# Kernel optimization log

Hardware: AMD Instinct MI355X
Metric: run time of the kernel (lower is better)

Reference implementation:

```python
import jax, jax.numpy as jnp
import numpy as np

N_NODES = 50000
N_EDGES = 800000
IN_CH = 128
HID_CH = 512
OUT_CH = 256


def setup_inputs() -> dict:
    key = jax.random.key(0)
    k1, k2, k3, k4, k5, k6 = jax.random.split(key, 6)
    x = jax.random.normal(k1, (N_NODES, IN_CH), dtype=jnp.float32)
    edge_index = jnp.stack([
        jax.random.randint(k2, (N_EDGES,), 0, N_NODES, dtype=jnp.int64),
        jax.random.randint(k3, (N_EDGES,), 0, N_NODES, dtype=jnp.int64),
    ], axis=0)
    # Xavier-uniform init as in MLP.reset_parameters
    lim1 = float(np.sqrt(6.0 / (IN_CH + HID_CH)))
    lim2 = float(np.sqrt(6.0 / (HID_CH + OUT_CH)))
    W1 = jax.random.uniform(k4, (IN_CH, HID_CH), jnp.float32, -lim1, lim1)
    b1 = jnp.zeros((HID_CH,), jnp.float32)
    W2 = jax.random.uniform(k5, (HID_CH, OUT_CH), jnp.float32, -lim2, lim2)
    return {"x": x, "edge_index": edge_index, "W1": W1, "b1": b1, "W2": W2}


def reference(x, edge_index, W1, b1, W2):
    src = edge_index[0]
    dst = edge_index[1]
    # AnisoConv (K=None): unweighted SpMM with adj.t() -> out[dst] += x[src]
    agg = jax.ops.segment_sum(x[src], dst, num_segments=N_NODES)  # [N, in_ch]
    h = agg + x  # residual add of x_r = x[:size[1]] = x
    # MLP: Linear(in, hidden, bias=True) -> Linear(hidden, out, bias=False)
    h = h @ W1 + b1
    h = h @ W2
    return h
```

## Files before the change

### kernel.cpp

```cpp
#include <hip/hip_runtime.h>

#define N_NODES 50000
#define N_EDGES 800000
#define IN_CH   128
#define HID_CH  512
#define OUT_CH  256

#define BKT_SHIFT 7
#define BKT_NODES 128
#define NBKT ((N_NODES + BKT_NODES - 1) / BKT_NODES)
#define BCAP 4096
#define P1_EPT    8
#define P1_EPB    (512 * P1_EPT)
#define P1_BLOCKS ((N_EDGES + P1_EPB - 1) / P1_EPB)
#define CVT_BLOCKS 3125

typedef __attribute__((ext_vector_type(8))) short bf16x8;
typedef __attribute__((ext_vector_type(4))) float f32x4;

static __device__ __forceinline__ ushort f2bf(float f) {
    uint u = __float_as_uint(f);
    uint r = u + 0x7fffu + ((u >> 16) & 1u);
    return (ushort)(r >> 16);
}

__global__ __launch_bounds__(1024) void build_w12(const float* __restrict__ W1,
                                                  const float* __restrict__ b1,
                                                  const float* __restrict__ W2,
                                                  ushort* __restrict__ W12t,
                                                  float* __restrict__ b2,
                                                  int* __restrict__ bucketcnt) {
    __shared__ float a[4][HID_CH];
    __shared__ float red[4][4][256];
    const int t   = threadIdx.x;
    const int j   = t & 255;
    const int kc  = t >> 8;
    const int blk = blockIdx.x;
    if (blk == 0 && t < NBKT) bucketcnt[t] = 0;

    const bool bias = (blk == 32);
    if (!bias) {
        const int i0 = blk * 4;
        for (int lin = t; lin < 4 * HID_CH; lin += 1024)
            a[lin >> 9][lin & 511] = W1[(size_t)(i0 + (lin >> 9)) * HID_CH + (lin & 511)];
    } else {
        for (int lin = t; lin < HID_CH; lin += 1024) a[0][lin] = b1[lin];
    }
    __syncthreads();

    float acc[4] = {0.f, 0.f, 0.f, 0.f};
    const int k0 = kc * 128;
    if (!bias) {
        for (int k = k0; k < k0 + 128; ++k) {
            const float w = W2[(size_t)k * OUT_CH + j];
#pragma unroll
            for (int r = 0; r < 4; ++r) acc[r] = fmaf(a[r][k], w, acc[r]);
        }
    } else {
        for (int k = k0; k < k0 + 128; ++k)
            acc[0] = fmaf(a[0][k], W2[(size_t)k * OUT_CH + j], acc[0]);
    }
#pragma unroll
    for (int r = 0; r < 4; ++r) red[kc][r][j] = acc[r];
    __syncthreads();
    if (kc == 0) {
#pragma unroll
        for (int r = 0; r < 4; ++r) {
            const float s = red[0][r][j] + red[1][r][j] + red[2][r][j] + red[3][r][j];
            if (!bias) W12t[(size_t)j * IN_CH + blk * 4 + r] = f2bf(s);
            else if (r == 0) b2[j] = s;
        }
    }
}

__global__ __launch_bounds__(512) void cvt_part(const float* __restrict__ x,
                                                ushort* __restrict__ xb,
                                                const int* __restrict__ ei,
                                                int* __restrict__ bucketcnt,
                                                uint* __restrict__ pairbuf) {
    __shared__ uint stage[P1_EPB];
    __shared__ int cnt[512], off[512], cur[512], base[512];
    const int t = threadIdx.x;

    if (blockIdx.x < CVT_BLOCKS) {
        const int gid = blockIdx.x * 512 + t;
        const float4 v = *(const float4*)(x + (size_t)gid * 4);
        ushort4 o;
        o.x = f2bf(v.x); o.y = f2bf(v.y); o.z = f2bf(v.z); o.w = f2bf(v.w);
        *(ushort4*)(xb + (size_t)gid * 4) = o;
        return;
    }

    const int e0 = (blockIdx.x - CVT_BLOCKS) * P1_EPB;

    cnt[t] = 0;
    __syncthreads();

    uint pk[P1_EPT];
    int  bk[P1_EPT];
    bool vl[P1_EPT];
#pragma unroll
    for (int i = 0; i < P1_EPT; ++i) {
        const int e = e0 + i * 512 + t;
        vl[i] = (e < N_EDGES);
        if (vl[i]) {
            const int src = ei[e];
            const int dst = ei[N_EDGES + e];
            const int b = dst >> BKT_SHIFT;
            bk[i] = b;
            pk[i] = ((uint)b << 23) | ((uint)src << 7) | (uint)(dst & (BKT_NODES - 1));
            atomicAdd(&cnt[b], 1);
        }
    }
    __syncthreads();

    off[t] = cnt[t];
    __syncthreads();
#pragma unroll
    for (int d = 1; d < 512; d <<= 1) {
        const int u = (t >= d) ? off[t - d] : 0;
        __syncthreads();
        off[t] += u;
        __syncthreads();
    }
    off[t] -= cnt[t];
    cur[t] = off[t];
    if (t < NBKT && cnt[t] > 0)
        base[t] = t * BCAP + atomicAdd(&bucketcnt[t], cnt[t]);
    __syncthreads();

#pragma unroll
    for (int i = 0; i < P1_EPT; ++i)
        if (vl[i]) {
            const int lp = atomicAdd(&cur[bk[i]], 1);
            stage[lp] = pk[i];
        }
    __syncthreads();

    const int TOT = off[511] + cnt[511];
    for (int idx = t; idx < TOT; idx += 512) {
        const uint p = stage[idx];
        const int b = (int)(p >> 23);
        pairbuf[base[b] + (idx - off[b])] = p;
    }
}

__global__ __launch_bounds__(256) void bucket_fill2(const uint* __restrict__ pairbuf,
                                                    const int* __restrict__ bucketcnt,
                                                    int* __restrict__ locrow,
                                                    int* __restrict__ srcidx) {
    __shared__ int cnt[128], off[128], cur[128];
    const int b = blockIdx.x;
    const int t = threadIdx.x;
    const int ne = bucketcnt[b];
    const uint* eb = pairbuf + (size_t)b * BCAP;

    if (t < 128) cnt[t] = 0;
    __syncthreads();
    for (int i = t; i < ne; i += 256)
        atomicAdd(&cnt[eb[i] & (BKT_NODES - 1)], 1);
    __syncthreads();

    if (t < 128) off[t] = cnt[t];
    __syncthreads();
#pragma unroll
    for (int d = 1; d < 128; d <<= 1) {
        int u = 0;
        if (t < 128 && t >= d) u = off[t - d];
        __syncthreads();
        if (t < 128 && t >= d) off[t] += u;
        __syncthreads();
    }
    if (t < 128) {
        off[t] -= cnt[t];
        cur[t] = off[t];
        locrow[b * (BKT_NODES + 1) + t] = off[t];
        if (t == 0) locrow[b * (BKT_NODES + 1) + BKT_NODES] = ne;
    }
    __syncthreads();

    for (int i = t; i < ne; i += 256) {
        const uint p = eb[i];
        const int ln  = (int)(p & (BKT_NODES - 1));
        const int src = (int)((p >> 7) & 0xFFFFu);
        const int pos = atomicAdd(&cur[ln], 1);
        srcidx[(size_t)b * BCAP + pos] = src;
    }
}

__global__ __launch_bounds__(256) void gather_bf16(const ushort* __restrict__ xb,
                                                   const int* __restrict__ locrow,
                                                   const int* __restrict__ srcidx,
                                                   ushort* __restrict__ aggb) {
    const int node = (int)((blockIdx.x * 256u + threadIdx.x) >> 6);
    const int lane = threadIdx.x & 63;
    if (node >= N_NODES) return;
    const int b  = node >> BKT_SHIFT;
    const int ln = node & (BKT_NODES - 1);
    const uint* xrow = (const uint*)xb;
    const uint self = xrow[(size_t)node * 64 + lane];
    float ax = __uint_as_float(self << 16);
    float ay = __uint_as_float(self & 0xffff0000u);
    int e = locrow[b * (BKT_NODES + 1) + ln];
    const int end = locrow[b * (BKT_NODES + 1) + ln + 1];
    const int* sb = srcidx + (size_t)b * BCAP;
    for (; e + 8 <= end; e += 8) {
        uint v[8];
#pragma unroll
        for (int i = 0; i < 8; ++i) {
            const int s = sb[e + i];
            v[i] = xrow[(size_t)s * 64 + lane];
        }
#pragma unroll
        for (int i = 0; i < 8; ++i) {
            ax += __uint_as_float(v[i] << 16);
            ay += __uint_as_float(v[i] & 0xffff0000u);
        }
    }
    for (; e < end; ++e) {
        const uint v = xrow[(size_t)sb[e] * 64 + lane];
        ax += __uint_as_float(v << 16); ay += __uint_as_float(v & 0xffff0000u);
    }
    const uint packed = ((uint)f2bf(ay) << 16) | (uint)f2bf(ax);
    ((uint*)aggb)[(size_t)node * 64 + lane] = packed;
}

__global__ __launch_bounds__(512) void mfma_gemm(const ushort* __restrict__ aggb,
                                                 const ushort* __restrict__ w12t,
                                                 const float* __restrict__ b2,
                                                 float* __restrict__ out) {
    __shared__ ushort bt[256 * 128];
    const int tid = threadIdx.x;

#pragma unroll
    for (int it = 0; it < 8; ++it) {
        const int i = tid + it * 512;
        const int n = i >> 4, s = i & 15;
        const uint4 v = *(const uint4*)(w12t + (size_t)i * 8);
        *(uint4*)(&bt[(n << 7) + ((s ^ (n & 7)) << 3)]) = v;
    }
    __syncthreads();

    const int lane = tid & 63;
    const int w    = tid >> 6;
    const int rbase = blockIdx.x * 128 + (w >> 1) * 32;
    const int cbase = (w & 1) * 128;
    const int l15 = lane & 15;
    const int oct = lane >> 4;

    f32x4 acc[2][8];
#pragma unroll
    for (int m = 0; m < 2; ++m)
#pragma unroll
        for (int n = 0; n < 8; ++n)
            acc[m][n] = (f32x4){0.f, 0.f, 0.f, 0.f};

#pragma unroll
    for (int kk = 0; kk < 4; ++kk) {
        bf16x8 afr[2];
#pragma unroll
        for (int m = 0; m < 2; ++m) {
            int row = rbase + m * 16 + l15;
            row = row < N_NODES ? row : N_NODES - 1;
            afr[m] = *(const bf16x8*)(aggb + (size_t)row * IN_CH + kk * 32 + oct * 8);
        }
#pragma unroll
        for (int n = 0; n < 8; ++n) {
            const int col  = cbase + n * 16 + l15;
            const int slot = (kk * 4 + oct) ^ (col & 7);
            const bf16x8 bfr = *(const bf16x8*)(&bt[(col << 7) + (slot << 3)]);
#pragma unroll
            for (int m = 0; m < 2; ++m)
                acc[m][n] = __builtin_amdgcn_mfma_f32_16x16x32_bf16(
                    afr[m], bfr, acc[m][n], 0, 0, 0);
        }
    }

#pragma unroll
    for (int m = 0; m < 2; ++m) {
        const int row0 = rbase + m * 16 + oct * 4;
#pragma unroll
        for (int n = 0; n < 8; ++n) {
            const int col = cbase + n * 16 + l15;
            const float bias = b2[col];
#pragma unroll
            for (int r = 0; r < 4; ++r) {
                const int row = row0 + r;
                if (row < N_NODES)
                    __builtin_nontemporal_store(acc[m][n][r] + bias,
                                                &out[(size_t)row * OUT_CH + col]);
            }
        }
    }
}

extern "C" void kernel_launch(void* const* d_in, const int* in_sizes, int n_in,
                              void* d_out, int out_size, void* d_ws, size_t ws_size,
                              hipStream_t stream) {
    const float* x  = (const float*)d_in[0];
    const int*   ei = (const int*)d_in[1];
    const float* W1 = (const float*)d_in[2];
    const float* b1 = (const float*)d_in[3];
    const float* W2 = (const float*)d_in[4];
    float* out = (float*)d_out;

    char* ws = (char*)d_ws;
    ushort* xb        = (ushort*)(ws + 0);
    ushort* aggb      = (ushort*)(ws + 12800000);
    uint*   pairbuf   = (uint*)  (ws + 12800000);
    ushort* W12t      = (ushort*)(ws + 25600000);
    float*  b2        = (float*) (ws + 25665536);
    int*    srcidx    = (int*)   (ws + 25666560);
    int*    locrow    = (int*)   (ws + 32072704);
    int*    bucketcnt = (int*)   (ws + 32274460);

    build_w12<<<dim3(33), dim3(1024), 0, stream>>>(W1, b1, W2, W12t, b2, bucketcnt);

    cvt_part<<<dim3(CVT_BLOCKS + P1_BLOCKS), dim3(512), 0, stream>>>(
        x, xb, ei, bucketcnt, pairbuf);

    bucket_fill2<<<dim3(NBKT), dim3(256), 0, stream>>>(pairbuf, bucketcnt,
                                                       locrow, srcidx);

    gather_bf16<<<dim3(N_NODES * 64 / 256), dim3(256), 0, stream>>>(
        xb, locrow, srcidx, aggb);

    mfma_gemm<<<dim3((N_NODES + 127) / 128), dim3(512), 0, stream>>>(
        aggb, W12t, b2, out);
}
```

Measured before the change: 93.57 us.

## Fuse bucket sort, neighbor gather and MFMA GEMM into one per-bucket kernel

Merges the per-bucket counting sort, the bf16 neighbor gather and the GEMM into a single kernel. Each 512-thread block sorts its bucket's source indices into LDS, gathers 128 aggregated rows into a swizzled LDS tile, and runs the MFMA GEMM straight from that tile. This removes two kernel launches and the global round trips for srcidx, locrow and the aggregated activations. In exchange, the B fragments are now read from global memory (W12t, 64KB, likely cache-resident) rather than staged in LDS, and the larger LDS footprint per block may lower occupancy.

```diff
diff --git a/kernel.cpp b/kernel.cpp
--- a/kernel.cpp
+++ b/kernel.cpp
@@ -145,22 +145,28 @@
     }
 }
 
-__global__ __launch_bounds__(256) void bucket_fill2(const uint* __restrict__ pairbuf,
+__global__ __launch_bounds__(512) void fused_bucket(const ushort* __restrict__ xb,
                                                     const int* __restrict__ bucketcnt,
-                                                    int* __restrict__ locrow,
-                                                    int* __restrict__ srcidx) {
-    __shared__ int cnt[128], off[128], cur[128];
+                                                    const uint* __restrict__ pairbuf,
+                                                    const ushort* __restrict__ w12t,
+                                                    const float* __restrict__ b2,
+                                                    float* __restrict__ out) {
+    __shared__ int  srcloc[BCAP];
+    __shared__ uint atile[BKT_NODES * 64];
+    __shared__ int  cnt[128], off[128], cur[128], locrow[129];
+
     const int b = blockIdx.x;
     const int t = threadIdx.x;
     const int ne = bucketcnt[b];
     const uint* eb = pairbuf + (size_t)b * BCAP;
+    const int nbase = b * BKT_NODES;
+    const int nloc = (nbase + BKT_NODES <= N_NODES) ? BKT_NODES : (N_NODES - nbase);
 
     if (t < 128) cnt[t] = 0;
     __syncthreads();
-    for (int i = t; i < ne; i += 256)
+    for (int i = t; i < ne; i += 512)
         atomicAdd(&cnt[eb[i] & (BKT_NODES - 1)], 1);
     __syncthreads();
-
     if (t < 128) off[t] = cnt[t];
     __syncthreads();
 #pragma unroll
@@ -174,77 +180,52 @@
     if (t < 128) {
         off[t] -= cnt[t];
         cur[t] = off[t];
-        locrow[b * (BKT_NODES + 1) + t] = off[t];
-        if (t == 0) locrow[b * (BKT_NODES + 1) + BKT_NODES] = ne;
-    }
-    __syncthreads();
-
-    for (int i = t; i < ne; i += 256) {
+        locrow[t] = off[t];
+        if (t == 0) locrow[128] = ne;
+    }
+    __syncthreads();
+    for (int i = t; i < ne; i += 512) {
         const uint p = eb[i];
-        const int ln  = (int)(p & (BKT_NODES - 1));
-        const int src = (int)((p >> 7) & 0xFFFFu);
+        const int ln = (int)(p & (BKT_NODES - 1));
         const int pos = atomicAdd(&cur[ln], 1);
-        srcidx[(size_t)b * BCAP + pos] = src;
-    }
-}
-
-__global__ __launch_bounds__(256) void gather_bf16(const ushort* __restrict__ xb,
-                                                   const int* __restrict__ locrow,
-                                                   const int* __restrict__ srcidx,
-                                                   ushort* __restrict__ aggb) {
-    const int node = (int)((blockIdx.x * 256u + threadIdx.x) >> 6);
-    const int lane = threadIdx.x & 63;
-    if (node >= N_NODES) return;
-    const int b  = node >> BKT_SHIFT;
-    const int ln = node & (BKT_NODES - 1);
+        srcloc[pos] = (int)((p >> 7) & 0xFFFFu);
+    }
+    __syncthreads();
+
+    const int lane = t & 63;
+    const int wv   = t >> 6;
     const uint* xrow = (const uint*)xb;
-    const uint self = xrow[(size_t)node * 64 + lane];
-    float ax = __uint_as_float(self << 16);
-    float ay = __uint_as_float(self & 0xffff0000u);
-    int e = locrow[b * (BKT_NODES + 1) + ln];
-    const int end = locrow[b * (BKT_NODES + 1) + ln + 1];
-    const int* sb = srcidx + (size_t)b * BCAP;
-    for (; e + 8 <= end; e += 8) {
-        uint v[8];
-#pragma unroll
-        for (int i = 0; i < 8; ++i) {
-            const int s = sb[e + i];
-            v[i] = xrow[(size_t)s * 64 + lane];
-        }
-#pragma unroll
-        for (int i = 0; i < 8; ++i) {
-            ax += __uint_as_float(v[i] << 16);
-            ay += __uint_as_float(v[i] & 0xffff0000u);
-        }
-    }
-    for (; e < end; ++e) {
-        const uint v = xrow[(size_t)sb[e] * 64 + lane];
-        ax += __uint_as_float(v << 16); ay += __uint_as_float(v & 0xffff0000u);
-    }
-    const uint packed = ((uint)f2bf(ay) << 16) | (uint)f2bf(ax);
-    ((uint*)aggb)[(size_t)node * 64 + lane] = packed;
-}
-
-__global__ __launch_bounds__(512) void mfma_gemm(const ushort* __restrict__ aggb,
-                                                 const ushort* __restrict__ w12t,
-                                                 const float* __restrict__ b2,
-                                                 float* __restrict__ out) {
-    __shared__ ushort bt[256 * 128];
-    const int tid = threadIdx.x;
-
-#pragma unroll
-    for (int it = 0; it < 8; ++it) {
-        const int i = tid + it * 512;
-        const int n = i >> 4, s = i & 15;
-        const uint4 v = *(const uint4*)(w12t + (size_t)i * 8);
-        *(uint4*)(&bt[(n << 7) + ((s ^ (n & 7)) << 3)]) = v;
-    }
-    __syncthreads();
-
-    const int lane = tid & 63;
-    const int w    = tid >> 6;
-    const int rbase = blockIdx.x * 128 + (w >> 1) * 32;
-    const int cbase = (w & 1) * 128;
+    for (int ln = wv; ln < nloc; ln += 8) {
+        const uint self = xrow[(size_t)(nbase + ln) * 64 + lane];
+        float ax = __uint_as_float(self << 16);
+        float ay = __uint_as_float(self & 0xffff0000u);
+        int e = locrow[ln];
+        const int end = locrow[ln + 1];
+        for (; e + 8 <= end; e += 8) {
+            uint v[8];
+#pragma unroll
+            for (int i = 0; i < 8; ++i) {
+                const int s = srcloc[e + i];
+                v[i] = xrow[(size_t)s * 64 + lane];
+            }
+#pragma unroll
+            for (int i = 0; i < 8; ++i) {
+                ax += __uint_as_float(v[i] << 16);
+                ay += __uint_as_float(v[i] & 0xffff0000u);
+            }
+        }
+        for (; e < end; ++e) {
+            const uint v = xrow[(size_t)srcloc[e] * 64 + lane];
+            ax += __uint_as_float(v << 16); ay += __uint_as_float(v & 0xffff0000u);
+        }
+        const int slot = (lane >> 2) ^ (ln & 7);
+        atile[ln * 64 + slot * 4 + (lane & 3)] =
+            ((uint)f2bf(ay) << 16) | (uint)f2bf(ax);
+    }
+    __syncthreads();
+
+    const int rbl  = (wv >> 1) * 32;
+    const int cbase = (wv & 1) * 128;
     const int l15 = lane & 15;
     const int oct = lane >> 4;
 
@@ -260,15 +241,15 @@
         bf16x8 afr[2];
 #pragma unroll
         for (int m = 0; m < 2; ++m) {
-            int row = rbase + m * 16 + l15;
-            row = row < N_NODES ? row : N_NODES - 1;
-            afr[m] = *(const bf16x8*)(aggb + (size_t)row * IN_CH + kk * 32 + oct * 8);
+            const int row = rbl + m * 16 + l15;
+            const int slot = (kk * 4 + oct) ^ (row & 7);
+            afr[m] = *(const bf16x8*)((const char*)atile + row * 256 + slot * 16);
         }
 #pragma unroll
         for (int n = 0; n < 8; ++n) {
-            const int col  = cbase + n * 16 + l15;
-            const int slot = (kk * 4 + oct) ^ (col & 7);
-            const bf16x8 bfr = *(const bf16x8*)(&bt[(col << 7) + (slot << 3)]);
+            const int col = cbase + n * 16 + l15;
+            const bf16x8 bfr = *(const bf16x8*)(w12t + (size_t)col * IN_CH
+                                                + kk * 32 + oct * 8);
 #pragma unroll
             for (int m = 0; m < 2; ++m)
                 acc[m][n] = __builtin_amdgcn_mfma_f32_16x16x32_bf16(
@@ -278,7 +259,7 @@
 
 #pragma unroll
     for (int m = 0; m < 2; ++m) {
-        const int row0 = rbase + m * 16 + oct * 4;
+        const int row0 = nbase + rbl + m * 16 + oct * 4;
 #pragma unroll
         for (int n = 0; n < 8; ++n) {
             const int col = cbase + n * 16 + l15;
@@ -306,25 +287,16 @@
 
     char* ws = (char*)d_ws;
     ushort* xb        = (ushort*)(ws + 0);
-    ushort* aggb      = (ushort*)(ws + 12800000);
-    uint*   pairbuf   = (uint*)  (ws + 12800000);
-    ushort* W12t      = (ushort*)(ws + 25600000);
-    float*  b2        = (float*) (ws + 25665536);
-    int*    srcidx    = (int*)   (ws + 25666560);
-    int*    locrow    = (int*)   (ws + 32072704);
-    int*    bucketcnt = (int*)   (ws + 32274460);
+    ushort* W12t      = (ushort*)(ws + 12800000);
+    float*  b2        = (float*) (ws + 12865536);
+    uint*   pairbuf   = (uint*)  (ws + 12866560);
+    int*    bucketcnt = (int*)   (ws + 19272704);
 
     build_w12<<<dim3(33), dim3(1024), 0, stream>>>(W1, b1, W2, W12t, b2, bucketcnt);
 
     cvt_part<<<dim3(CVT_BLOCKS + P1_BLOCKS), dim3(512), 0, stream>>>(
         x, xb, ei, bucketcnt, pairbuf);
 
-    bucket_fill2<<<dim3(NBKT), dim3(256), 0, stream>>>(pairbuf, bucketcnt,
-                                                       locrow, srcidx);
-
-    gather_bf16<<<dim3(N_NODES * 64 / 256), dim3(256), 0, stream>>>(
-        xb, locrow, srcidx, aggb);
-
-    mfma_gemm<<<dim3((N_NODES + 127) / 128), dim3(512), 0, stream>>>(
-        aggb, W12t, b2, out);
-}
+    fused_bucket<<<dim3(NBKT), dim3(512), 0, stream>>>(
+        xb, bucketcnt, pairbuf, W12t, b2, out);
+}
```

Measured after the change: 137.9 us. 1.47x slower.
